# Performance work log

Hardware: AMD Instinct MI355X
Metric: run time of the kernel (lower is better)

Reference implementation:

```python
import jax, jax.numpy as jnp
import numpy as np

N_NODES = 100000
N_EDGES = 1600000
IN_FEATS = 128
OUT_FEATS = 128


def setup_inputs() -> dict:
    key = jax.random.key(0)
    k1, k2, k3, k4, k5 = jax.random.split(key, 5)
    feature = jax.random.normal(k1, (N_NODES, IN_FEATS), dtype=jnp.float32)
    src = jax.random.randint(k2, (N_EDGES,), 0, N_NODES, dtype=jnp.int64)
    dst = jax.random.randint(k3, (N_EDGES,), 0, N_NODES, dtype=jnp.int64)
    # nn.Linear default init: U(-1/sqrt(in), 1/sqrt(in)); randn scaled is fine for a numeric baseline
    bound = 1.0 / np.sqrt(IN_FEATS)
    W = jax.random.uniform(k4, (OUT_FEATS, IN_FEATS), dtype=jnp.float32, minval=-bound, maxval=bound)
    b = jax.random.uniform(k5, (OUT_FEATS,), dtype=jnp.float32, minval=-bound, maxval=bound)
    return {"feature": feature, "src": src, "dst": dst, "W": W, "b": b}


def reference(feature, src, dst, W, b):
    # message passing: copy source feature along each edge, sum into destination node
    agg = jax.ops.segment_sum(feature[src], dst, num_segments=N_NODES)  # [N, in_feats]
    # node apply: ReLU(Linear(h))
    return jax.nn.relu(agg @ W.T + b)  # [N, out_feats]
```

## Files before the change

kernel.cpp:

```cpp
#include <hip/hip_runtime.h>

#define N_NODES 100000
#define N_EDGES 1600000
#define F 128

#define NB    1563
#define NBP2  2048
#define CAP   1280
#define CHUNK 8192
#define BCUR  1599

#define BIN_BLOCKS   196
#define HGEMM_BLOCKS 782
#define FRONT_GRID_LIN (BIN_BLOCKS + HGEMM_BLOCKS)
#define ACC_GRID     1024

#define LDP  136
#define SMEM_BYTES 77824

typedef __bf16  bf16x8 __attribute__((ext_vector_type(8)));
typedef float   f32x4  __attribute__((ext_vector_type(4)));

__device__ inline unsigned short f32_to_bf16(float f) {
    unsigned u = __builtin_bit_cast(unsigned, f);
    u += 0x7FFFu + ((u >> 16) & 1u);
    return (unsigned short)(u >> 16);
}
__device__ inline unsigned pack_bf16x2(float lo, float hi) {
    return (unsigned)f32_to_bf16(lo) | ((unsigned)f32_to_bf16(hi) << 16);
}
__device__ inline void addrow(float* acc, const uint4 v) {
    acc[0] += __builtin_bit_cast(float, v.x << 16);
    acc[1] += __builtin_bit_cast(float, v.x & 0xFFFF0000u);
    acc[2] += __builtin_bit_cast(float, v.y << 16);
    acc[3] += __builtin_bit_cast(float, v.y & 0xFFFF0000u);
    acc[4] += __builtin_bit_cast(float, v.z << 16);
    acc[5] += __builtin_bit_cast(float, v.z & 0xFFFF0000u);
    acc[6] += __builtin_bit_cast(float, v.w << 16);
    acc[7] += __builtin_bit_cast(float, v.w & 0xFFFF0000u);
}

__global__ __launch_bounds__(1024) void gcn_front_lin(
    const float* __restrict__ feat, const float* __restrict__ W,
    const int* __restrict__ src, const int* __restrict__ dst,
    int* __restrict__ gcur, unsigned* __restrict__ bins,
    unsigned short* __restrict__ H)
{
    __shared__ __align__(16) unsigned char smem[SMEM_BYTES];

    const int tid = threadIdx.x;
    const int bx  = blockIdx.x;

    if (bx >= BIN_BLOCKS) {
        unsigned short* Alds = (unsigned short*)smem;
        unsigned short* Wlds = Alds + 128 * LDP;
        const int row0 = (bx - BIN_BLOCKS) * 128;

        #pragma unroll
        for (int i = 0; i < 4; ++i) {
            const int c = tid + i * 1024;
            const int r = c >> 5, cc = c & 31;
            const f32x4 v = *(const f32x4*)(W + (size_t)c * 4);
            uint2 p; p.x = pack_bf16x2(v[0], v[1]); p.y = pack_bf16x2(v[2], v[3]);
            *(uint2*)&Wlds[r * LDP + cc * 4] = p;
        }
        #pragma unroll
        for (int i = 0; i < 4; ++i) {
            const int c = tid + i * 1024;
            const int r = c >> 5, cc = c & 31;
            int gr = row0 + r; if (gr > N_NODES - 1) gr = N_NODES - 1;
            const f32x4 v = __builtin_nontemporal_load(
                                 (const f32x4*)(feat + (size_t)gr * F + cc * 4));
            uint2 p; p.x = pack_bf16x2(v[0], v[1]); p.y = pack_bf16x2(v[2], v[3]);
            *(uint2*)&Alds[r * LDP + cc * 4] = p;
        }
        __syncthreads();

        const int lane = tid & 63, wv = tid >> 6;
        const int lr = lane & 15, lq = lane >> 4;
        const int wr = wv & 7;
        const int wc = wv >> 3;

        f32x4 acc[4] = {};
        #pragma unroll
        for (int kk = 0; kk < 4; ++kk) {
            const bf16x8 a = __builtin_bit_cast(bf16x8,
                *(const uint4*)&Alds[(wr * 16 + lr) * LDP + kk * 32 + lq * 8]);
            #pragma unroll
            for (int n2 = 0; n2 < 4; ++n2) {
                const bf16x8 w = __builtin_bit_cast(bf16x8,
                    *(const uint4*)&Wlds[((wc * 4 + n2) * 16 + lr) * LDP + kk * 32 + lq * 8]);
                acc[n2] = __builtin_amdgcn_mfma_f32_16x16x32_bf16(a, w, acc[n2], 0, 0, 0);
            }
        }
        __syncthreads();

        #pragma unroll
        for (int rg = 0; rg < 4; ++rg) {
            const int r = wr * 16 + lq * 4 + rg;
            #pragma unroll
            for (int n2 = 0; n2 < 4; ++n2)
                Alds[r * LDP + (wc * 4 + n2) * 16 + lr] = f32_to_bf16(acc[n2][rg]);
        }
        __syncthreads();

        #pragma unroll
        for (int i = 0; i < 2; ++i) {
            const int c = tid + i * 1024;
            const int r = c >> 4, cc = c & 15;
            const int gr = row0 + r;
            if (gr < N_NODES)
                *(uint4*)(H + (size_t)gr * F + cc * 8) = *(const uint4*)&Alds[r * LDP + cc * 8];
        }
        return;
    }

    unsigned*       cnt    = (unsigned*)smem;
    unsigned*       off    = cnt + NBP2;
    int*            gbase  = (int*)(off + NBP2);
    unsigned*       staged = (unsigned*)(gbase + NBP2);
    unsigned short* sbk    = (unsigned short*)(staged + CHUNK);
    unsigned*       scan   = (unsigned*)(sbk + CHUNK);

    const int e0 = bx * CHUNK;

    #pragma unroll
    for (int i = 0; i < 2; ++i) cnt[tid + i * 1024] = 0;
    __syncthreads();

    int sv[8], dv[8];
    #pragma unroll
    for (int i = 0; i < 8; ++i) {
        const int e = e0 + tid + i * 1024;
        if (e < N_EDGES) {
            sv[i] = src[e];
            dv[i] = dst[e];
            atomicAdd(&cnt[dv[i] >> 6], 1u);
        } else dv[i] = -1;
    }
    __syncthreads();

    const int lane = tid & 63, wid = tid >> 6;
    const unsigned s = cnt[2 * tid] + cnt[2 * tid + 1];
    unsigned v = s;
    #pragma unroll
    for (int o = 1; o < 64; o <<= 1) {
        const unsigned t = __shfl_up(v, o, 64);
        if (lane >= o) v += t;
    }
    if (lane == 63) scan[wid] = v;
    __syncthreads();
    if (tid < 16) {
        const unsigned w = scan[tid];
        unsigned x = w;
        #pragma unroll
        for (int o = 1; o < 16; o <<= 1) {
            const unsigned t = __shfl_up(x, o, 16);
            if (tid >= o) x += t;
        }
        scan[tid] = x - w;
        if (tid == 15) scan[16] = x;
    }
    __syncthreads();
    const unsigned incl = v + scan[wid];
    const unsigned run  = incl - s;
    off[2 * tid]     = run;
    off[2 * tid + 1] = run + cnt[2 * tid];
    __syncthreads();

    #pragma unroll
    for (int i = 0; i < 8; ++i) {
        if (dv[i] >= 0) {
            const int bk = dv[i] >> 6;
            const unsigned w = (unsigned)sv[i] | ((unsigned)(dv[i] & 63) << 17);
            const unsigned p = atomicAdd(&off[bk], 1u);
            staged[p] = w;
            sbk[p] = (unsigned short)bk;
        }
    }
    __syncthreads();

    #pragma unroll
    for (int i = 0; i < 2; ++i) {
        const int bk = 2 * tid + i;
        if (bk < NB && cnt[bk] > 0)
            gbase[bk] = atomicAdd(&gcur[bk], (int)cnt[bk]);
    }
    __syncthreads();

    const int c_tot = (int)scan[16];
    for (int p = tid; p < c_tot; p += 1024) {
        const int bk = sbk[p];
        const int gp = gbase[bk] + (p - (int)(off[bk] - cnt[bk]));
        if (gp < CAP) bins[(size_t)bk * CAP + gp] = staged[p];
    }
}

__global__ __launch_bounds__(512) void gcn_accum_lin(
    int* __restrict__ gcur,
    const unsigned* __restrict__ bins,
    const unsigned short* __restrict__ H,
    const float* __restrict__ b,
    float* __restrict__ out)
{
    __shared__ unsigned tmp[CAP];
    __shared__ unsigned list[CAP];
    __shared__ int cnt64[64], pos64[64], cur64[64];
    __shared__ int sbkt;
    __shared__ int nextn;

    const int tid  = threadIdx.x;
    const int lane = tid & 63;
    const int sl   = tid & 15;

    const f32x4 b0 = *(const f32x4*)(b + sl * 8);
    const f32x4 b1 = *(const f32x4*)(b + sl * 8 + 4);

    for (;;) {
        __syncthreads();
        if (tid == 0) {
            sbkt  = atomicAdd(&gcur[BCUR], 1);
            nextn = 0;
        }
        __syncthreads();
        const int bkt = sbkt;
        if (bkt >= NB) return;

        int c = gcur[bkt]; if (c > CAP) c = CAP;
        const unsigned* bb = bins + (size_t)bkt * CAP;

        for (int i = tid; i < c; i += 512)
            tmp[i] = __builtin_nontemporal_load(bb + i);
        if (tid < 64) cnt64[tid] = 0;
        __syncthreads();

        for (int i = tid; i < c; i += 512) atomicAdd(&cnt64[(tmp[i] >> 17) & 63], 1);
        __syncthreads();

        if (tid < 64) {
            const int cv = cnt64[tid];
            int x = cv;
            #pragma unroll
            for (int o = 1; o < 64; o <<= 1) {
                const int t = __shfl_up(x, o, 64);
                if (tid >= o) x += t;
            }
            pos64[tid] = x - cv;
            cur64[tid] = x - cv;
        }
        __syncthreads();

        for (int i = tid; i < c; i += 512) {
            const unsigned w = tmp[i];
            const int p = atomicAdd(&cur64[(w >> 17) & 63], 1);
            list[p] = w;
        }
        __syncthreads();

        const int n0 = bkt * 64;

        for (;;) {
            int myn = 0;
            if (sl == 0) myn = atomicAdd(&nextn, 1);
            myn = __shfl(myn, lane & 48, 64);
            if (myn >= 64) break;

            const int st = pos64[myn];
            const int en = st + cnt64[myn];

            float a0[8] = {0,0,0,0,0,0,0,0};
            float a1[8] = {0,0,0,0,0,0,0,0};
            int k = st;
            for (; k + 7 < en; k += 8) {
                const unsigned w0 = list[k],     w1 = list[k + 1];
                const unsigned w2 = list[k + 2], w3 = list[k + 3];
                const unsigned w4 = list[k + 4], w5 = list[k + 5];
                const unsigned w6 = list[k + 6], w7 = list[k + 7];
                const uint4 v0 = *(const uint4*)(H + (size_t)(w0 & 0x1FFFF) * F + sl * 8);
                const uint4 v1 = *(const uint4*)(H + (size_t)(w1 & 0x1FFFF) * F + sl * 8);
                const uint4 v2 = *(const uint4*)(H + (size_t)(w2 & 0x1FFFF) * F + sl * 8);
                const uint4 v3 = *(const uint4*)(H + (size_t)(w3 & 0x1FFFF) * F + sl * 8);
                const uint4 v4 = *(const uint4*)(H + (size_t)(w4 & 0x1FFFF) * F + sl * 8);
                const uint4 v5 = *(const uint4*)(H + (size_t)(w5 & 0x1FFFF) * F + sl * 8);
                const uint4 v6 = *(const uint4*)(H + (size_t)(w6 & 0x1FFFF) * F + sl * 8);
                const uint4 v7 = *(const uint4*)(H + (size_t)(w7 & 0x1FFFF) * F + sl * 8);
                addrow(a0, v0); addrow(a1, v1); addrow(a0, v2); addrow(a1, v3);
                addrow(a0, v4); addrow(a1, v5); addrow(a0, v6); addrow(a1, v7);
            }
            for (; k + 3 < en; k += 4) {
                const unsigned w0 = list[k],     w1 = list[k + 1];
                const unsigned w2 = list[k + 2], w3 = list[k + 3];
                const uint4 v0 = *(const uint4*)(H + (size_t)(w0 & 0x1FFFF) * F + sl * 8);
                const uint4 v1 = *(const uint4*)(H + (size_t)(w1 & 0x1FFFF) * F + sl * 8);
                const uint4 v2 = *(const uint4*)(H + (size_t)(w2 & 0x1FFFF) * F + sl * 8);
                const uint4 v3 = *(const uint4*)(H + (size_t)(w3 & 0x1FFFF) * F + sl * 8);
                addrow(a0, v0); addrow(a1, v1); addrow(a0, v2); addrow(a1, v3);
            }
            for (; k < en; ++k) {
                const unsigned w0 = list[k];
                const uint4 v0 = *(const uint4*)(H + (size_t)(w0 & 0x1FFFF) * F + sl * 8);
                addrow(a0, v0);
            }
            #pragma unroll
            for (int q = 0; q < 8; ++q) a0[q] += a1[q];

            const int n = n0 + myn;
            if (n < N_NODES) {
                f32x4 o0, o1;
                o0[0] = fmaxf(a0[0] + b0[0], 0.0f);
                o0[1] = fmaxf(a0[1] + b0[1], 0.0f);
                o0[2] = fmaxf(a0[2] + b0[2], 0.0f);
                o0[3] = fmaxf(a0[3] + b0[3], 0.0f);
                o1[0] = fmaxf(a0[4] + b1[0], 0.0f);
                o1[1] = fmaxf(a0[5] + b1[1], 0.0f);
                o1[2] = fmaxf(a0[6] + b1[2], 0.0f);
                o1[3] = fmaxf(a0[7] + b1[3], 0.0f);
                float* orow = out + (size_t)n * F + sl * 8;
                __builtin_nontemporal_store(o0, (f32x4*)orow);
                __builtin_nontemporal_store(o1, (f32x4*)(orow + 4));
            }
        }
    }
}

#define FEAT_BLOCKS 3125
#define WCONV_BLOCKS 16
#define FRONT_GRID  (BIN_BLOCKS + FEAT_BLOCKS + WCONV_BLOCKS)

__global__ __launch_bounds__(1024) void gcn_front(
    const float* __restrict__ feat, const float* __restrict__ W,
    const int* __restrict__ src, const int* __restrict__ dst,
    int* __restrict__ gcur, unsigned* __restrict__ bins,
    unsigned short* __restrict__ Wbf, float* __restrict__ out)
{
    __shared__ unsigned cnt[NBP2];
    __shared__ unsigned off[NBP2];
    __shared__ int      gbase[NBP2];
    __shared__ unsigned staged[CHUNK];
    __shared__ unsigned short sbk[CHUNK];
    __shared__ unsigned scan[1024];

    const int tid = threadIdx.x;
    const int bx  = blockIdx.x;

    if (bx >= BIN_BLOCKS) {
        const int rb = bx - BIN_BLOCKS;
        if (rb < FEAT_BLOCKS) {
            const int t = rb * 1024 + tid;
            const float4 v = *(const float4*)(feat + (size_t)t * 4);
            uint2 p;
            p.x = pack_bf16x2(v.x, v.y);
            p.y = pack_bf16x2(v.z, v.w);
            const int n = t >> 5, q = t & 31;
            *(uint2*)((char*)out + (size_t)n * 512 + q * 8) = p;
        } else {
            const int i = (rb - FEAT_BLOCKS) * 1024 + tid;
            Wbf[i] = f32_to_bf16(W[i]);
        }
        return;
    }

    const int e0 = bx * CHUNK;

    #pragma unroll
    for (int i = 0; i < 2; ++i) cnt[tid + i * 1024] = 0;
    __syncthreads();

    int sv[8], dv[8];
    #pragma unroll
    for (int i = 0; i < 8; ++i) {
        const int e = e0 + tid + i * 1024;
        if (e < N_EDGES) {
            sv[i] = src[e];
            dv[i] = dst[e];
            atomicAdd(&cnt[dv[i] >> 6], 1u);
        } else dv[i] = -1;
    }
    __syncthreads();

    const unsigned s = cnt[2 * tid] + cnt[2 * tid + 1];
    scan[tid] = s;
    __syncthreads();
    for (int o = 1; o < 1024; o <<= 1) {
        const unsigned t = (tid >= o) ? scan[tid - o] : 0;
        __syncthreads();
        scan[tid] += t;
        __syncthreads();
    }
    const unsigned run = scan[tid] - s;
    off[2 * tid]     = run;
    off[2 * tid + 1] = run + cnt[2 * tid];
    __syncthreads();

    #pragma unroll
    for (int i = 0; i < 8; ++i) {
        if (dv[i] >= 0) {
            const int bk = dv[i] >> 6;
            const unsigned w = (unsigned)sv[i] | ((unsigned)(dv[i] & 63) << 17);
            const unsigned p = atomicAdd(&off[bk], 1u);
            staged[p] = w;
            sbk[p] = (unsigned short)bk;
        }
    }
    __syncthreads();

    #pragma unroll
    for (int i = 0; i < 2; ++i) {
        const int bk = 2 * tid + i;
        if (bk < NB && cnt[bk] > 0)
            gbase[bk] = atomicAdd(&gcur[bk], (int)cnt[bk]);
    }
    __syncthreads();

    const int c_tot = (int)scan[1023];
    for (int p = tid; p < c_tot; p += 1024) {
        const int bk = sbk[p];
        const int gp = gbase[bk] + (p - (int)(off[bk] - cnt[bk]));
        if (gp < CAP) bins[(size_t)bk * CAP + gp] = staged[p];
    }
}

__global__ __launch_bounds__(512) void gcn_accum2(
    const int* __restrict__ gcur,
    const unsigned* __restrict__ bins,
    float* __restrict__ out)
{
    __shared__ unsigned tmp[CAP];
    __shared__ unsigned list[CAP];
    __shared__ int cnt64[64], scn[64], pos64[64], cur64[64];

    const int tid = threadIdx.x;
    const int bkt = blockIdx.x;

    int c = gcur[bkt]; if (c > CAP) c = CAP;
    const unsigned* bb = bins + (size_t)bkt * CAP;

    for (int i = tid; i < c; i += 512) tmp[i] = bb[i];
    if (tid < 64) cnt64[tid] = 0;
    __syncthreads();

    for (int i = tid; i < c; i += 512) atomicAdd(&cnt64[(tmp[i] >> 17) & 63], 1);
    __syncthreads();

    if (tid < 64) scn[tid] = cnt64[tid];
    __syncthreads();
    #pragma unroll
    for (int o = 1; o < 64; o <<= 1) {
        int t = 0;
        if (tid < 64 && tid >= o) t = scn[tid - o];
        __syncthreads();
        if (tid < 64) scn[tid] += t;
        __syncthreads();
    }
    if (tid < 64) {
        const int st = scn[tid] - cnt64[tid];
        pos64[tid] = st;
        cur64[tid] = st;
    }
    __syncthreads();

    for (int i = tid; i < c; i += 512) {
        const unsigned w = tmp[i];
        const int p = atomicAdd(&cur64[(w >> 17) & 63], 1);
        list[p] = w;
    }
    __syncthreads();

    const int grp = tid >> 4;
    const int sl  = tid & 15;
    const int n0  = bkt * 64;

    #pragma unroll
    for (int ni = 0; ni < 2; ++ni) {
        const int l  = grp * 2 + ni;
        const int st = pos64[l];
        const int en = st + cnt64[l];

        float a0[8] = {0,0,0,0,0,0,0,0};
        float a1[8] = {0,0,0,0,0,0,0,0};
        int k = st;
        for (; k + 3 < en; k += 4) {
            const unsigned w0 = list[k],     w1 = list[k + 1];
            const unsigned w2 = list[k + 2], w3 = list[k + 3];
            const uint4 v0 = *(const uint4*)((const char*)out + (size_t)(w0 & 0x1FFFF) * 512 + sl * 16);
            const uint4 v1 = *(const uint4*)((const char*)out + (size_t)(w1 & 0x1FFFF) * 512 + sl * 16);
            const uint4 v2 = *(const uint4*)((const char*)out + (size_t)(w2 & 0x1FFFF) * 512 + sl * 16);
            const uint4 v3 = *(const uint4*)((const char*)out + (size_t)(w3 & 0x1FFFF) * 512 + sl * 16);
            addrow(a0, v0); addrow(a1, v1); addrow(a0, v2); addrow(a1, v3);
        }
        for (; k < en; ++k) {
            const unsigned w0 = list[k];
            const uint4 v0 = *(const uint4*)((const char*)out + (size_t)(w0 & 0x1FFFF) * 512 + sl * 16);
            addrow(a0, v0);
        }
        #pragma unroll
        for (int q = 0; q < 8; ++q) a0[q] += a1[q];

        const int n = n0 + l;
        if (n < N_NODES) {
            uint4 o;
            o.x = pack_bf16x2(a0[0], a0[1]);
            o.y = pack_bf16x2(a0[2], a0[3]);
            o.z = pack_bf16x2(a0[4], a0[5]);
            o.w = pack_bf16x2(a0[6], a0[7]);
            *(uint4*)((char*)out + (size_t)n * 512 + 256 + sl * 16) = o;
        }
    }
}

#define MT   128

__global__ __launch_bounds__(256) void gcn_gemm_mfma(
    float* __restrict__ out,
    const unsigned short* __restrict__ Wbf,
    const float* __restrict__ b)
{
    __shared__ unsigned short Alds[MT * LDP];
    __shared__ unsigned short Wlds[F * LDP];

    const int tid  = threadIdx.x;
    const int row0 = blockIdx.x * MT;

    #pragma unroll
    for (int i = 0; i < 8; ++i) {
        const int c = tid + i * 256;
        const int r = c >> 4, cc = c & 15;
        *(uint4*)&Wlds[r * LDP + cc * 8] = *(const uint4*)&Wbf[c * 8];
    }
    #pragma unroll
    for (int i = 0; i < 8; ++i) {
        const int c = tid + i * 256;
        const int r = c >> 4, cc = c & 15;
        int gr = row0 + r; if (gr > N_NODES - 1) gr = N_NODES - 1;
        const uint4 v = *(const uint4*)((const char*)out + (size_t)gr * 512 + 256 + cc * 16);
        *(uint4*)&Alds[r * LDP + cc * 8] = v;
    }
    __syncthreads();

    const int lane = tid & 63;
    const int wv   = tid >> 6;
    const int lr   = lane & 15;
    const int lq   = lane >> 4;

    f32x4 acc[2][8] = {};
    #pragma unroll
    for (int kk = 0; kk < 4; ++kk) {
        bf16x8 a[2], w[8];
        #pragma unroll
        for (int i = 0; i < 2; ++i)
            a[i] = __builtin_bit_cast(bf16x8,
                *(const uint4*)&Alds[(wv * 32 + i * 16 + lr) * LDP + kk * 32 + lq * 8]);
        #pragma unroll
        for (int n = 0; n < 8; ++n)
            w[n] = __builtin_bit_cast(bf16x8,
                *(const uint4*)&Wlds[(n * 16 + lr) * LDP + kk * 32 + lq * 8]);
        #pragma unroll
        for (int i = 0; i < 2; ++i)
            #pragma unroll
            for (int n = 0; n < 8; ++n)
                acc[i][n] = __builtin_amdgcn_mfma_f32_16x16x32_bf16(a[i], w[n], acc[i][n], 0, 0, 0);
    }

    float bias[8];
    #pragma unroll
    for (int n = 0; n < 8; ++n) bias[n] = b[n * 16 + lr];

    #pragma unroll
    for (int i = 0; i < 2; ++i) {
        const int rbase = wv * 32 + i * 16 + lq * 4;
        #pragma unroll
        for (int rg = 0; rg < 4; ++rg) {
            const int gr = row0 + rbase + rg;
            if (gr < N_NODES) {
                float* orow = out + (size_t)gr * F;
                #pragma unroll
                for (int n = 0; n < 8; ++n) {
                    const float v = acc[i][n][rg] + bias[n];
                    orow[n * 16 + lr] = v > 0.0f ? v : 0.0f;
                }
            }
        }
    }
}

__global__ __launch_bounds__(256) void gcn_scatter(
    const float* __restrict__ feat,
    const int* __restrict__ src, const int* __restrict__ dst,
    float* __restrict__ agg)
{
    const int sub  = threadIdx.x >> 5;
    const int lane = threadIdx.x & 31;
    const long long e = (long long)blockIdx.x * 8 + sub;
    if (e >= N_EDGES) return;
    const int s = src[e], d = dst[e];
    const float4 v = *(const float4*)(feat + (size_t)s * F + lane * 4);
    float* ar = agg + (size_t)d * F + lane * 4;
    unsafeAtomicAdd(ar + 0, v.x);
    unsafeAtomicAdd(ar + 1, v.y);
    unsafeAtomicAdd(ar + 2, v.z);
    unsafeAtomicAdd(ar + 3, v.w);
}

#define GR  64
#define LDW 132
__global__ __launch_bounds__(256) void gcn_gemm_relu(
    float* __restrict__ agg_out,
    const float* __restrict__ W, const float* __restrict__ b)
{
    __shared__ float Wl[F][LDW];
    __shared__ float At[GR][LDW];
    const int tid = threadIdx.x;
    const long long row0 = (long long)blockIdx.x * GR;
    #pragma unroll
    for (int i = 0; i < 64; ++i) {
        const int e = tid + i * 256;
        Wl[e >> 7][e & 127] = W[e];
    }
    #pragma unroll
    for (int i = 0; i < 32; ++i) {
        const int e = tid + i * 256;
        const int r = e >> 7, k2 = e & 127;
        const long long gr = row0 + r;
        At[r][k2] = (gr < N_NODES) ? agg_out[gr * F + k2] : 0.0f;
    }
    __syncthreads();
    const int tx = tid & 15, ty = tid >> 4, r0 = ty * 4;
    float acc[4][8];
    #pragma unroll
    for (int r = 0; r < 4; ++r)
        #pragma unroll
        for (int m = 0; m < 8; ++m) acc[r][m] = 0.0f;
    for (int k0 = 0; k0 < F; k0 += 4) {
        float4 a[4], w[8];
        #pragma unroll
        for (int r = 0; r < 4; ++r) a[r] = *(const float4*)&At[r0 + r][k0];
        #pragma unroll
        for (int m = 0; m < 8; ++m) w[m] = *(const float4*)&Wl[tx + 16 * m][k0];
        #pragma unroll
        for (int r = 0; r < 4; ++r)
            #pragma unroll
            for (int m = 0; m < 8; ++m)
                acc[r][m] += a[r].x * w[m].x + a[r].y * w[m].y
                           + a[r].z * w[m].z + a[r].w * w[m].w;
    }
    float bias[8];
    #pragma unroll
    for (int m = 0; m < 8; ++m) bias[m] = b[tx + 16 * m];
    __syncthreads();
    #pragma unroll
    for (int r = 0; r < 4; ++r) {
        const long long gr = row0 + r0 + r;
        if (gr < N_NODES) {
            float* orow = agg_out + gr * F;
            #pragma unroll
            for (int m = 0; m < 8; ++m) {
                const float v = acc[r][m] + bias[m];
                orow[tx + 16 * m] = v > 0.0f ? v : 0.0f;
            }
        }
    }
}

extern "C" void kernel_launch(void* const* d_in, const int* in_sizes, int n_in,
                              void* d_out, int out_size, void* d_ws, size_t ws_size,
                              hipStream_t stream) {
    const float* feat = (const float*)d_in[0];
    const int*   src  = (const int*)d_in[1];
    const int*   dst  = (const int*)d_in[2];
    const float* W    = (const float*)d_in[3];
    const float* b    = (const float*)d_in[4];
    float* out = (float*)d_out;

    const size_t ws_lin = 1600u * 4 + (size_t)NB * CAP * 4 + (size_t)N_NODES * F * 2;
    const size_t ws_old = 1600u * 4 + (size_t)NB * CAP * 4 + (size_t)F * F * 2;

    if (ws_size >= ws_lin) {
        int* gcur = (int*)d_ws;
        unsigned* bins = (unsigned*)(gcur + 1600);
        unsigned short* H = (unsigned short*)(bins + (size_t)NB * CAP);

        hipMemsetAsync(gcur, 0, 1600 * sizeof(int), stream);
        gcn_front_lin<<<FRONT_GRID_LIN, 1024, 0, stream>>>(feat, W, src, dst, gcur, bins, H);
        gcn_accum_lin<<<ACC_GRID, 512, 0, stream>>>(gcur, bins, H, b, out);
    } else if (ws_size >= ws_old) {
        int* gcur = (int*)d_ws;
        unsigned* bins = (unsigned*)(gcur + 1600);
        unsigned short* Wbf = (unsigned short*)(bins + (size_t)NB * CAP);

        hipMemsetAsync(gcur, 0, NB * sizeof(int), stream);
        gcn_front   <<<FRONT_GRID, 1024, 0, stream>>>(feat, W, src, dst, gcur, bins, Wbf, out);
        gcn_accum2  <<<NB, 512, 0, stream>>>(gcur, bins, out);
        gcn_gemm_mfma<<<(N_NODES + MT - 1) / MT, 256, 0, stream>>>(out, Wbf, b);
    } else {
        hipMemsetAsync(out, 0, (size_t)N_NODES * F * sizeof(float), stream);
        gcn_scatter<<<N_EDGES / 8, 256, 0, stream>>>(feat, src, dst, out);
        gcn_gemm_relu<<<(N_NODES + GR - 1) / GR, 256, 0, stream>>>(out, W, b);
    }
}
```

Before: 195.8 us.

## Split fused front kernel into separate init, bin, and GEMM launches

The fused front kernel, which ran edge binning and the feature-times-W GEMM as different block roles in one grid, becomes separate launches. A small init kernel converts W to bf16 and zeroes the counters in place of the memset. The accumulate kernel drops its persistent atomic work-stealing loop and uses one block per bucket. Nontemporal loads and stores become normal ones. This trades the overlap of binning with the GEMM, and dynamic load balancing, for simpler kernels with better occupancy, at the cost of extra launch overhead and serialization.

```diff
diff --git a/kernel.cpp b/kernel.cpp
--- a/kernel.cpp
+++ b/kernel.cpp
@@ -8,15 +8,11 @@
 #define NBP2  2048
 #define CAP   1280
 #define CHUNK 8192
-#define BCUR  1599
 
 #define BIN_BLOCKS   196
 #define HGEMM_BLOCKS 782
-#define FRONT_GRID_LIN (BIN_BLOCKS + HGEMM_BLOCKS)
-#define ACC_GRID     1024
 
 #define LDP  136
-#define SMEM_BYTES 77824
 
 typedef __bf16  bf16x8 __attribute__((ext_vector_type(8)));
 typedef float   f32x4  __attribute__((ext_vector_type(4)));
@@ -40,89 +36,28 @@
     acc[7] += __builtin_bit_cast(float, v.w & 0xFFFF0000u);
 }
 
-__global__ __launch_bounds__(1024) void gcn_front_lin(
-    const float* __restrict__ feat, const float* __restrict__ W,
+__global__ __launch_bounds__(1024) void gcn_init(
+    const float* __restrict__ W, unsigned short* __restrict__ Wbf,
+    int* __restrict__ gcur)
+{
+    const int i = blockIdx.x * 1024 + threadIdx.x;
+    Wbf[i] = f32_to_bf16(W[i]);
+    if (i < 1600) gcur[i] = 0;
+}
+
+__global__ __launch_bounds__(1024) void gcn_bin(
     const int* __restrict__ src, const int* __restrict__ dst,
-    int* __restrict__ gcur, unsigned* __restrict__ bins,
-    unsigned short* __restrict__ H)
-{
-    __shared__ __align__(16) unsigned char smem[SMEM_BYTES];
+    int* __restrict__ gcur, unsigned* __restrict__ bins)
+{
+    __shared__ unsigned cnt[NBP2];
+    __shared__ unsigned off[NBP2];
+    __shared__ int      gbase[NBP2];
+    __shared__ unsigned staged[CHUNK];
+    __shared__ unsigned short sbk[CHUNK];
+    __shared__ unsigned scan[32];
 
     const int tid = threadIdx.x;
-    const int bx  = blockIdx.x;
-
-    if (bx >= BIN_BLOCKS) {
-        unsigned short* Alds = (unsigned short*)smem;
-        unsigned short* Wlds = Alds + 128 * LDP;
-        const int row0 = (bx - BIN_BLOCKS) * 128;
-
-        #pragma unroll
-        for (int i = 0; i < 4; ++i) {
-            const int c = tid + i * 1024;
-            const int r = c >> 5, cc = c & 31;
-            const f32x4 v = *(const f32x4*)(W + (size_t)c * 4);
-            uint2 p; p.x = pack_bf16x2(v[0], v[1]); p.y = pack_bf16x2(v[2], v[3]);
-            *(uint2*)&Wlds[r * LDP + cc * 4] = p;
-        }
-        #pragma unroll
-        for (int i = 0; i < 4; ++i) {
-            const int c = tid + i * 1024;
-            const int r = c >> 5, cc = c & 31;
-            int gr = row0 + r; if (gr > N_NODES - 1) gr = N_NODES - 1;
-            const f32x4 v = __builtin_nontemporal_load(
-                                 (const f32x4*)(feat + (size_t)gr * F + cc * 4));
-            uint2 p; p.x = pack_bf16x2(v[0], v[1]); p.y = pack_bf16x2(v[2], v[3]);
-            *(uint2*)&Alds[r * LDP + cc * 4] = p;
-        }
-        __syncthreads();
-
-        const int lane = tid & 63, wv = tid >> 6;
-        const int lr = lane & 15, lq = lane >> 4;
-        const int wr = wv & 7;
-        const int wc = wv >> 3;
-
-        f32x4 acc[4] = {};
-        #pragma unroll
-        for (int kk = 0; kk < 4; ++kk) {
-            const bf16x8 a = __builtin_bit_cast(bf16x8,
-                *(const uint4*)&Alds[(wr * 16 + lr) * LDP + kk * 32 + lq * 8]);
-            #pragma unroll
-            for (int n2 = 0; n2 < 4; ++n2) {
-                const bf16x8 w = __builtin_bit_cast(bf16x8,
-                    *(const uint4*)&Wlds[((wc * 4 + n2) * 16 + lr) * LDP + kk * 32 + lq * 8]);
-                acc[n2] = __builtin_amdgcn_mfma_f32_16x16x32_bf16(a, w, acc[n2], 0, 0, 0);
-            }
-        }
-        __syncthreads();
-
-        #pragma unroll
-        for (int rg = 0; rg < 4; ++rg) {
-            const int r = wr * 16 + lq * 4 + rg;
-            #pragma unroll
-            for (int n2 = 0; n2 < 4; ++n2)
-                Alds[r * LDP + (wc * 4 + n2) * 16 + lr] = f32_to_bf16(acc[n2][rg]);
-        }
-        __syncthreads();
-
-        #pragma unroll
-        for (int i = 0; i < 2; ++i) {
-            const int c = tid + i * 1024;
-            const int r = c >> 4, cc = c & 15;
-            const int gr = row0 + r;
-            if (gr < N_NODES)
-                *(uint4*)(H + (size_t)gr * F + cc * 8) = *(const uint4*)&Alds[r * LDP + cc * 8];
-        }
-        return;
-    }
-
-    unsigned*       cnt    = (unsigned*)smem;
-    unsigned*       off    = cnt + NBP2;
-    int*            gbase  = (int*)(off + NBP2);
-    unsigned*       staged = (unsigned*)(gbase + NBP2);
-    unsigned short* sbk    = (unsigned short*)(staged + CHUNK);
-    unsigned*       scan   = (unsigned*)(sbk + CHUNK);
-
-    const int e0 = bx * CHUNK;
+    const int e0  = blockIdx.x * CHUNK;
 
     #pragma unroll
     for (int i = 0; i < 2; ++i) cnt[tid + i * 1024] = 0;
@@ -196,8 +131,73 @@
     }
 }
 
+__global__ __launch_bounds__(1024) void gcn_hgemm(
+    const float* __restrict__ feat, const unsigned short* __restrict__ Wbf,
+    unsigned short* __restrict__ H)
+{
+    __shared__ unsigned short Alds[128 * LDP];
+    __shared__ unsigned short Wlds[128 * LDP];
+
+    const int tid  = threadIdx.x;
+    const int row0 = blockIdx.x * 128;
+
+    #pragma unroll
+    for (int i = 0; i < 2; ++i) {
+        const int c = tid + i * 1024;
+        const int r = c >> 4, cc = c & 15;
+        *(uint4*)&Wlds[r * LDP + cc * 8] = *(const uint4*)&Wbf[c * 8];
+    }
+    #pragma unroll
+    for (int i = 0; i < 4; ++i) {
+        const int c = tid + i * 1024;
+        const int r = c >> 5, cc = c & 31;
+        int gr = row0 + r; if (gr > N_NODES - 1) gr = N_NODES - 1;
+        const f32x4 v = *(const f32x4*)(feat + (size_t)gr * F + cc * 4);
+        uint2 p; p.x = pack_bf16x2(v[0], v[1]); p.y = pack_bf16x2(v[2], v[3]);
+        *(uint2*)&Alds[r * LDP + cc * 4] = p;
+    }
+    __syncthreads();
+
+    const int lane = tid & 63, wv = tid >> 6;
+    const int lr = lane & 15, lq = lane >> 4;
+    const int wr = wv & 7;
+    const int wc = wv >> 3;
+
+    f32x4 acc[4] = {};
+    #pragma unroll
+    for (int kk = 0; kk < 4; ++kk) {
+        const bf16x8 a = __builtin_bit_cast(bf16x8,
+            *(const uint4*)&Alds[(wr * 16 + lr) * LDP + kk * 32 + lq * 8]);
+        #pragma unroll
+        for (int n2 = 0; n2 < 4; ++n2) {
+            const bf16x8 w = __builtin_bit_cast(bf16x8,
+                *(const uint4*)&Wlds[((wc * 4 + n2) * 16 + lr) * LDP + kk * 32 + lq * 8]);
+            acc[n2] = __builtin_amdgcn_mfma_f32_16x16x32_bf16(a, w, acc[n2], 0, 0, 0);
+        }
+    }
+    __syncthreads();
+
+    #pragma unroll
+    for (int rg = 0; rg < 4; ++rg) {
+        const int r = wr * 16 + lq * 4 + rg;
+        #pragma unroll
+        for (int n2 = 0; n2 < 4; ++n2)
+            Alds[r * LDP + (wc * 4 + n2) * 16 + lr] = f32_to_bf16(acc[n2][rg]);
+    }
+    __syncthreads();
+
+    #pragma unroll
+    for (int i = 0; i < 2; ++i) {
+        const int c = tid + i * 1024;
+        const int r = c >> 4, cc = c & 15;
+        const int gr = row0 + r;
+        if (gr < N_NODES)
+            *(uint4*)(H + (size_t)gr * F + cc * 8) = *(const uint4*)&Alds[r * LDP + cc * 8];
+    }
+}
+
 __global__ __launch_bounds__(512) void gcn_accum_lin(
-    int* __restrict__ gcur,
+    const int* __restrict__ gcur,
     const unsigned* __restrict__ bins,
     const unsigned short* __restrict__ H,
     const float* __restrict__ b,
@@ -206,119 +206,108 @@
     __shared__ unsigned tmp[CAP];
     __shared__ unsigned list[CAP];
     __shared__ int cnt64[64], pos64[64], cur64[64];
-    __shared__ int sbkt;
     __shared__ int nextn;
 
     const int tid  = threadIdx.x;
+    const int bkt  = blockIdx.x;
     const int lane = tid & 63;
     const int sl   = tid & 15;
 
+    int c = gcur[bkt]; if (c > CAP) c = CAP;
+    const unsigned* bb = bins + (size_t)bkt * CAP;
+
+    for (int i = tid; i < c; i += 512) tmp[i] = bb[i];
+    if (tid < 64) cnt64[tid] = 0;
+    if (tid == 0) nextn = 0;
+    __syncthreads();
+
+    for (int i = tid; i < c; i += 512) atomicAdd(&cnt64[(tmp[i] >> 17) & 63], 1);
+    __syncthreads();
+
+    if (tid < 64) {
+        const int cv = cnt64[tid];
+        int x = cv;
+        #pragma unroll
+        for (int o = 1; o < 64; o <<= 1) {
+            const int t = __shfl_up(x, o, 64);
+            if (tid >= o) x += t;
+        }
+        pos64[tid] = x - cv;
+        cur64[tid] = x - cv;
+    }
+    __syncthreads();
+
+    for (int i = tid; i < c; i += 512) {
+        const unsigned w = tmp[i];
+        const int p = atomicAdd(&cur64[(w >> 17) & 63], 1);
+        list[p] = w;
+    }
+    __syncthreads();
+
+    const int n0 = bkt * 64;
+
     const f32x4 b0 = *(const f32x4*)(b + sl * 8);
     const f32x4 b1 = *(const f32x4*)(b + sl * 8 + 4);
 
     for (;;) {
-        __syncthreads();
-        if (tid == 0) {
-            sbkt  = atomicAdd(&gcur[BCUR], 1);
-            nextn = 0;
-        }
-        __syncthreads();
-        const int bkt = sbkt;
-        if (bkt >= NB) return;
-
-        int c = gcur[bkt]; if (c > CAP) c = CAP;
-        const unsigned* bb = bins + (size_t)bkt * CAP;
-
-        for (int i = tid; i < c; i += 512)
-            tmp[i] = __builtin_nontemporal_load(bb + i);
-        if (tid < 64) cnt64[tid] = 0;
-        __syncthreads();
-
-        for (int i = tid; i < c; i += 512) atomicAdd(&cnt64[(tmp[i] >> 17) & 63], 1);
-        __syncthreads();
-
-        if (tid < 64) {
-            const int cv = cnt64[tid];
-            int x = cv;
-            #pragma unroll
-            for (int o = 1; o < 64; o <<= 1) {
-                const int t = __shfl_up(x, o, 64);
-                if (tid >= o) x += t;
-            }
-            pos64[tid] = x - cv;
-            cur64[tid] = x - cv;
-        }
-        __syncthreads();
-
-        for (int i = tid; i < c; i += 512) {
-            const unsigned w = tmp[i];
-            const int p = atomicAdd(&cur64[(w >> 17) & 63], 1);
-            list[p] = w;
-        }
-        __syncthreads();
-
-        const int n0 = bkt * 64;
-
-        for (;;) {
-            int myn = 0;
-            if (sl == 0) myn = atomicAdd(&nextn, 1);
-            myn = __shfl(myn, lane & 48, 64);
-            if (myn >= 64) break;
-
-            const int st = pos64[myn];
-            const int en = st + cnt64[myn];
-
-            float a0[8] = {0,0,0,0,0,0,0,0};
-            float a1[8] = {0,0,0,0,0,0,0,0};
-            int k = st;
-            for (; k + 7 < en; k += 8) {
-                const unsigned w0 = list[k],     w1 = list[k + 1];
-                const unsigned w2 = list[k + 2], w3 = list[k + 3];
-                const unsigned w4 = list[k + 4], w5 = list[k + 5];
-                const unsigned w6 = list[k + 6], w7 = list[k + 7];
-                const uint4 v0 = *(const uint4*)(H + (size_t)(w0 & 0x1FFFF) * F + sl * 8);
-                const uint4 v1 = *(const uint4*)(H + (size_t)(w1 & 0x1FFFF) * F + sl * 8);
-                const uint4 v2 = *(const uint4*)(H + (size_t)(w2 & 0x1FFFF) * F + sl * 8);
-                const uint4 v3 = *(const uint4*)(H + (size_t)(w3 & 0x1FFFF) * F + sl * 8);
-                const uint4 v4 = *(const uint4*)(H + (size_t)(w4 & 0x1FFFF) * F + sl * 8);
-                const uint4 v5 = *(const uint4*)(H + (size_t)(w5 & 0x1FFFF) * F + sl * 8);
-                const uint4 v6 = *(const uint4*)(H + (size_t)(w6 & 0x1FFFF) * F + sl * 8);
-                const uint4 v7 = *(const uint4*)(H + (size_t)(w7 & 0x1FFFF) * F + sl * 8);
-                addrow(a0, v0); addrow(a1, v1); addrow(a0, v2); addrow(a1, v3);
-                addrow(a0, v4); addrow(a1, v5); addrow(a0, v6); addrow(a1, v7);
-            }
-            for (; k + 3 < en; k += 4) {
-                const unsigned w0 = list[k],     w1 = list[k + 1];
-                const unsigned w2 = list[k + 2], w3 = list[k + 3];
-                const uint4 v0 = *(const uint4*)(H + (size_t)(w0 & 0x1FFFF) * F + sl * 8);
-                const uint4 v1 = *(const uint4*)(H + (size_t)(w1 & 0x1FFFF) * F + sl * 8);
-                const uint4 v2 = *(const uint4*)(H + (size_t)(w2 & 0x1FFFF) * F + sl * 8);
-                const uint4 v3 = *(const uint4*)(H + (size_t)(w3 & 0x1FFFF) * F + sl * 8);
-                addrow(a0, v0); addrow(a1, v1); addrow(a0, v2); addrow(a1, v3);
-            }
-            for (; k < en; ++k) {
-                const unsigned w0 = list[k];
-                const uint4 v0 = *(const uint4*)(H + (size_t)(w0 & 0x1FFFF) * F + sl * 8);
-                addrow(a0, v0);
-            }
-            #pragma unroll
-            for (int q = 0; q < 8; ++q) a0[q] += a1[q];
-
-            const int n = n0 + myn;
-            if (n < N_NODES) {
-                f32x4 o0, o1;
-                o0[0] = fmaxf(a0[0] + b0[0], 0.0f);
-                o0[1] = fmaxf(a0[1] + b0[1], 0.0f);
-                o0[2] = fmaxf(a0[2] + b0[2], 0.0f);
-                o0[3] = fmaxf(a0[3] + b0[3], 0.0f);
-                o1[0] = fmaxf(a0[4] + b1[0], 0.0f);
-                o1[1] = fmaxf(a0[5] + b1[1], 0.0f);
-                o1[2] = fmaxf(a0[6] + b1[2], 0.0f);
-                o1[3] = fmaxf(a0[7] + b1[3], 0.0f);
-                float* orow = out + (size_t)n * F + sl * 8;
-                __builtin_nontemporal_store(o0, (f32x4*)orow);
-                __builtin_nontemporal_store(o1, (f32x4*)(orow + 4));
-            }
+        int myn = 0;
+        if (sl == 0) myn = atomicAdd(&nextn, 1);
+        myn = __shfl(myn, lane & 48, 64);
+        if (myn >= 64) break;
+
+        const int st = pos64[myn];
+        const int en = st + cnt64[myn];
+
+        float a0[8] = {0,0,0,0,0,0,0,0};
+        float a1[8] = {0,0,0,0,0,0,0,0};
+        int k = st;
+        for (; k + 7 < en; k += 8) {
+            const unsigned w0 = list[k],     w1 = list[k + 1];
+            const unsigned w2 = list[k + 2], w3 = list[k + 3];
+            const unsigned w4 = list[k + 4], w5 = list[k + 5];
+            const unsigned w6 = list[k + 6], w7 = list[k + 7];
+            const uint4 v0 = *(const uint4*)(H + (size_t)(w0 & 0x1FFFF) * F + sl * 8);
+            const uint4 v1 = *(const uint4*)(H + (size_t)(w1 & 0x1FFFF) * F + sl * 8);
+            const uint4 v2 = *(const uint4*)(H + (size_t)(w2 & 0x1FFFF) * F + sl * 8);
+            const uint4 v3 = *(const uint4*)(H + (size_t)(w3 & 0x1FFFF) * F + sl * 8);
+            const uint4 v4 = *(const uint4*)(H + (size_t)(w4 & 0x1FFFF) * F + sl * 8);
+            const uint4 v5 = *(const uint4*)(H + (size_t)(w5 & 0x1FFFF) * F + sl * 8);
+            const uint4 v6 = *(const uint4*)(H + (size_t)(w6 & 0x1FFFF) * F + sl * 8);
+            const uint4 v7 = *(const uint4*)(H + (size_t)(w7 & 0x1FFFF) * F + sl * 8);
+            addrow(a0, v0); addrow(a1, v1); addrow(a0, v2); addrow(a1, v3);
+            addrow(a0, v4); addrow(a1, v5); addrow(a0, v6); addrow(a1, v7);
+        }
+        for (; k + 3 < en; k += 4) {
+            const unsigned w0 = list[k],     w1 = list[k + 1];
+            const unsigned w2 = list[k + 2], w3 = list[k + 3];
+            const uint4 v0 = *(const uint4*)(H + (size_t)(w0 & 0x1FFFF) * F + sl * 8);
+            const uint4 v1 = *(const uint4*)(H + (size_t)(w1 & 0x1FFFF) * F + sl * 8);
+            const uint4 v2 = *(const uint4*)(H + (size_t)(w2 & 0x1FFFF) * F + sl * 8);
+            const uint4 v3 = *(const uint4*)(H + (size_t)(w3 & 0x1FFFF) * F + sl * 8);
+            addrow(a0, v0); addrow(a1, v1); addrow(a0, v2); addrow(a1, v3);
+        }
+        for (; k < en; ++k) {
+            const unsigned w0 = list[k];
+            const uint4 v0 = *(const uint4*)(H + (size_t)(w0 & 0x1FFFF) * F + sl * 8);
+            addrow(a0, v0);
+        }
+        #pragma unroll
+        for (int q = 0; q < 8; ++q) a0[q] += a1[q];
+
+        const int n = n0 + myn;
+        if (n < N_NODES) {
+            f32x4 o0, o1;
+            o0[0] = fmaxf(a0[0] + b0[0], 0.0f);
+            o0[1] = fmaxf(a0[1] + b0[1], 0.0f);
+            o0[2] = fmaxf(a0[2] + b0[2], 0.0f);
+            o0[3] = fmaxf(a0[3] + b0[3], 0.0f);
+            o1[0] = fmaxf(a0[4] + b1[0], 0.0f);
+            o1[1] = fmaxf(a0[5] + b1[1], 0.0f);
+            o1[2] = fmaxf(a0[6] + b1[2], 0.0f);
+            o1[3] = fmaxf(a0[7] + b1[3], 0.0f);
+            float* orow = out + (size_t)n * F + sl * 8;
+            *(f32x4*)orow = o0;
+            *(f32x4*)(orow + 4) = o1;
         }
     }
 }
@@ -671,17 +660,20 @@
     const float* b    = (const float*)d_in[4];
     float* out = (float*)d_out;
 
-    const size_t ws_lin = 1600u * 4 + (size_t)NB * CAP * 4 + (size_t)N_NODES * F * 2;
+    const size_t ws_lin = 1600u * 4 + (size_t)NB * CAP * 4
+                        + (size_t)N_NODES * F * 2 + (size_t)F * F * 2;
     const size_t ws_old = 1600u * 4 + (size_t)NB * CAP * 4 + (size_t)F * F * 2;
 
     if (ws_size >= ws_lin) {
         int* gcur = (int*)d_ws;
         unsigned* bins = (unsigned*)(gcur + 1600);
         unsigned short* H = (unsigned short*)(bins + (size_t)NB * CAP);
-
-        hipMemsetAsync(gcur, 0, 1600 * sizeof(int), stream);
-        gcn_front_lin<<<FRONT_GRID_LIN, 1024, 0, stream>>>(feat, W, src, dst, gcur, bins, H);
-        gcn_accum_lin<<<ACC_GRID, 512, 0, stream>>>(gcur, bins, H, b, out);
+        unsigned short* Wbf = H + (size_t)N_NODES * F;
+
+        gcn_init     <<<16, 1024, 0, stream>>>(W, Wbf, gcur);
+        gcn_bin      <<<BIN_BLOCKS, 1024, 0, stream>>>(src, dst, gcur, bins);
+        gcn_hgemm    <<<HGEMM_BLOCKS, 1024, 0, stream>>>(feat, Wbf, H);
+        gcn_accum_lin<<<NB, 512, 0, stream>>>(gcur, bins, H, b, out);
     } else if (ws_size >= ws_old) {
         int* gcur = (int*)d_ws;
         unsigned* bins = (unsigned*)(gcur + 1600);
```

Measured after the change: 194.5 us. Within noise of the previous version (-0.7%).
